# Performance work log

Measured on AMD Instinct MI355X. Metric: run time of the kernel, lower is better.

## Reference

```python
import jax, jax.numpy as jnp
import numpy as np

N, E, H, G, NF, L = 50000, 600000, 128, 50, 128, 6
NC, NM = 500, 100  # conformers, molecules
CUTOFF = 10.0
OFFSET = jnp.linspace(0.0, CUTOFF, G)                 # GaussianSmearing offsets
COEFF = -0.5 / (CUTOFF / (G - 1)) ** 2
LOG2 = float(np.log(2.0))

def ssp(x):  # ShiftedSoftplus
    return jax.nn.softplus(x) - LOG2

def setup_inputs() -> dict:
    key = jax.random.key(0)
    ks = jax.random.split(key, 24)
    s = 0.05
    return {
        'z': jax.random.randint(ks[0], (N,), 0, 120),
        'pos': jax.random.normal(ks[1], (N, 3), jnp.float32) * 5.0,
        'edge_row': jax.random.randint(ks[2], (E,), 0, N),   # source j
        'edge_col': jax.random.randint(ks[3], (E,), 0, N),   # target i
        'atom_to_conf': jnp.sort(jax.random.randint(ks[4], (N,), 0, NC)),
        'conf_to_mol': jnp.sort(jax.random.randint(ks[5], (NC,), 0, NM)),
        'emb_table': jax.random.normal(ks[6], (120, H)) * s,
        'mlp_w1': jax.random.normal(ks[7], (L, G, NF)) * s,
        'mlp_b1': jnp.zeros((L, NF)),
        'mlp_w2': jax.random.normal(ks[8], (L, NF, NF)) * s,
        'mlp_b2': jnp.zeros((L, NF)),
        'conv_lin1_w': jax.random.normal(ks[9], (L, H, NF)) * s,
        'conv_lin2_w': jax.random.normal(ks[10], (L, NF, H)) * s,
        'conv_lin2_b': jnp.zeros((L, H)),
        'int_lin_w': jax.random.normal(ks[11], (L, H, H)) * s,
        'int_lin_b': jnp.zeros((L, H)),
        'lin1_w': jax.random.normal(ks[12], (H, H)) * s,
        'lin1_b': jnp.zeros((H,)),
        'lin2_w': jax.random.normal(ks[13], (H, H)) * s,
        'lin2_b': jnp.zeros((H,)),
        'head_w1': jax.random.normal(ks[14], (H, H // 2)) * s,
        'head_b1': jnp.zeros((H // 2,)),
        'head_w2': jax.random.normal(ks[15], (H // 2, 1)) * s,
        'head_b2': jnp.zeros((1,)),
    }

def reference(z, pos, edge_row, edge_col, atom_to_conf, conf_to_mol,
              emb_table, mlp_w1, mlp_b1, mlp_w2, mlp_b2,
              conv_lin1_w, conv_lin2_w, conv_lin2_b, int_lin_w, int_lin_b,
              lin1_w, lin1_b, lin2_w, lin2_b,
              head_w1, head_b1, head_w2, head_b2):
    h = emb_table[z]                                         # [N,H]
    # edge geometry (radius graph distances)
    d = jnp.linalg.norm(pos[edge_row] - pos[edge_col], axis=-1)       # [E]
    edge_attr = jnp.exp(COEFF * (d[:, None] - OFFSET[None, :]) ** 2)  # [E,G]
    C = 0.5 * (jnp.cos(d * jnp.pi / CUTOFF) + 1.0)                    # [E]
    for i in range(L):
        # filter network + cosine cutoff
        W = ssp(edge_attr @ mlp_w1[i] + mlp_b1[i]) @ mlp_w2[i] + mlp_b2[i]
        W = W * C[:, None]                                   # [E,NF]
        xf = h @ conv_lin1_w[i]                              # [N,NF]
        msg = xf[edge_row] * W                               # gather x_j, multiply
        agg = jax.ops.segment_sum(msg, edge_col, num_segments=N)  # scatter-add
        x = agg @ conv_lin2_w[i] + conv_lin2_b[i]
        x = ssp(x) @ int_lin_w[i] + int_lin_b[i]
        h = h + x                                            # residual
    h = ssp(h @ lin1_w + lin1_b) @ lin2_w + lin2_b           # [N,H]
    conf_emb = jax.ops.segment_sum(h, atom_to_conf, num_segments=NC)  # [NC,H]
    mol_emb = jax.ops.segment_sum(conf_emb, conf_to_mol, num_segments=NM)  # [NM,H]
    out = (ssp(mol_emb @ head_w1 + head_b1) @ head_w2 + head_b2)[:, 0]  # [NM]
    return out
```

## Files before the change

kernel.cpp:

```cpp
#include <hip/hip_runtime.h>
#include <hip/hip_bf16.h>
#include <hip/hip_fp16.h>
#include <math.h>

#define H_DIM   128
#define NF_DIM  128
#define G_DIM   50
#define L_LAYERS 6
#define TBL     4096
#define DMAX    12.8f
#define CUTOFF_C 10.0f
#define COEFF_C (-0.5f * 49.0f * 49.0f / 100.0f)
#define SCAN_B  256
#define T_PER   16
#define STG_STR 140

typedef __bf16 bf16x8 __attribute__((ext_vector_type(8)));
typedef float  f32x4  __attribute__((ext_vector_type(4)));

__device__ __forceinline__ float sspf(float x) {
    float e = __expf(-fabsf(x));
    return fmaxf(x, 0.0f) + __logf(1.0f + e) - 0.69314718055994530942f;
}

__device__ __forceinline__ unsigned short f2bf(float f) {
    unsigned int u = __float_as_uint(f);
    u = (u + 0x7fffu + ((u >> 16) & 1u)) >> 16;
    return (unsigned short)u;
}

__device__ __forceinline__ float bf2f(unsigned short u) {
    return __uint_as_float(((unsigned int)u) << 16);
}

__device__ __forceinline__ int swz(int c) {
    return c ^ ((c >> 3) & 7) ^ ((c >> 8) & 3);
}

__global__ __launch_bounds__(128) void bt_sy(
        const float* __restrict__ w1, const float* __restrict__ b1,
        unsigned short* __restrict__ syb) {
    int l  = blockIdx.x / (TBL / T_PER);
    int t0 = (blockIdx.x % (TBL / T_PER)) * T_PER;
    int f  = threadIdx.x;
    __shared__ float sW1[G_DIM * 128];
    __shared__ float gs[T_PER][G_DIM + 2];
    for (int i = f; i < G_DIM * 128; i += 128)
        sW1[i] = w1[(size_t)l * G_DIM * 128 + i];
    if (f < G_DIM) {
        float o = f * (CUTOFF_C / (G_DIM - 1));
#pragma unroll
        for (int u = 0; u < T_PER; ++u) {
            float dt = (t0 + u) * (DMAX / (TBL - 1));
            float dd = dt - o;
            gs[u][f] = __expf(COEFF_C * dd * dd);
        }
    }
    __syncthreads();
    float y[T_PER];
    float bb = b1[l * 128 + f];
#pragma unroll
    for (int u = 0; u < T_PER; ++u) y[u] = bb;
    for (int g = 0; g < G_DIM; ++g) {
        float wv = sW1[g * 128 + f];
#pragma unroll
        for (int u = 0; u < T_PER; ++u) y[u] += gs[u][g] * wv;
    }
#pragma unroll
    for (int u = 0; u < T_PER; ++u)
        syb[((size_t)l * TBL + t0 + u) * 128 + f] = f2bf(sspf(y[u]));
}

__global__ __launch_bounds__(256, 4) void bt_gemm(
        const unsigned short* __restrict__ syb, const unsigned short* __restrict__ w2sw,
        const float* __restrict__ b2, unsigned short* __restrict__ tabb) {
    int l  = blockIdx.x >> 6;
    int m0 = (blockIdx.x & 63) * 64;
    const unsigned short* A = syb + (size_t)l * TBL * 128;
    const unsigned short* Bsw = w2sw + (size_t)l * 16384;
    const float* bias = b2 + l * 128;
    unsigned short* outp = tabb + (size_t)l * TBL * 128;

    __shared__ __align__(16) unsigned short frag[8192];
    __shared__ __align__(16) unsigned short stg[64 * STG_STR];
    int tid = threadIdx.x;
    for (int i = tid; i < 1024; i += 256) {
        int ks = i >> 8, w_ = (i >> 6) & 3, ln_ = i & 63;
        int row = m0 + w_ * 16 + (ln_ & 15);
        int kb = ks * 32 + (ln_ >> 4) * 8;
        uint4 v = *(const uint4*)(A + (size_t)row * 128 + kb);
        *(uint4*)(frag + swz(i) * 8) = v;
    }
    __syncthreads();
    int w = tid >> 6, ln = tid & 63;
    int quad = ln >> 4, l15 = ln & 15;
    f32x4 acc[8] = {};
#pragma unroll
    for (int ks = 0; ks < 4; ++ks) {
        bf16x8 af = *(const bf16x8*)(frag + swz((ks * 4 + w) * 64 + ln) * 8);
#pragma unroll
        for (int j = 0; j < 8; ++j) {
            bf16x8 bf = *(const bf16x8*)(Bsw + (((ks * 8 + j) * 64) + ln) * 8);
            acc[j] = __builtin_amdgcn_mfma_f32_16x16x32_bf16(af, bf, acc[j], 0, 0, 0);
        }
    }
#pragma unroll
    for (int j = 0; j < 8; ++j) {
        int col = j * 16 + l15;
        float bv = bias[col];
#pragma unroll
        for (int r = 0; r < 4; ++r)
            stg[(w * 16 + quad * 4 + r) * STG_STR + col] = f2bf(acc[j][r] + bv);
    }
    __syncthreads();
    for (int i = tid; i < 2048; i += 256) {
        int row = i >> 5, c4 = (i & 31) * 4;
        ushort4 s4 = *(const ushort4*)(stg + row * STG_STR + c4);
        *(uint2*)(outp + (size_t)(m0 + row) * 128 + c4) = *(const uint2*)&s4;
    }
}

__global__ __launch_bounds__(256) void embed_kernel(
        const int* __restrict__ z, const float* __restrict__ emb,
        unsigned short* __restrict__ hb, int N) {
    int idx = blockIdx.x * blockDim.x + threadIdx.x;
    if (idx >= N * H_DIM) return;
    int n = idx >> 7, f = idx & 127;
    hb[idx] = f2bf(emb[z[n] * H_DIM + f]);
}

__global__ __launch_bounds__(256) void prep_wt_all(
        const float* __restrict__ c1w, const float* __restrict__ c2w,
        const float* __restrict__ iw, const float* __restrict__ l1w,
        const float* __restrict__ w2, unsigned short* __restrict__ Bsw) {
    int m = blockIdx.x;
    const float* src = (m < 6)  ? c1w + (size_t)m * 16384
                     : (m < 12) ? c2w + (size_t)(m - 6) * 16384
                     : (m < 18) ? iw  + (size_t)(m - 12) * 16384
                     : (m == 18) ? l1w
                                 : w2 + (size_t)(m - 19) * 16384;
    unsigned short* dst = Bsw + (size_t)m * 16384;
    for (int i = threadIdx.x; i < 16384; i += 256) {
        int jj = i & 7, lane = (i >> 3) & 63, j = (i >> 9) & 7, ks = i >> 12;
        int n = j * 16 + (lane & 15);
        int k = ks * 32 + ((lane >> 4) & 3) * 8 + jj;
        dst[i] = f2bf(src[k * 128 + n]);
    }
}

__global__ __launch_bounds__(256) void count_kernel(
        const int* __restrict__ ec, int* __restrict__ cnt,
        int* __restrict__ rank, int E) {
    int e = blockIdx.x * blockDim.x + threadIdx.x;
    if (e < E) rank[e] = atomicAdd(&cnt[ec[e]], 1);
}

__global__ __launch_bounds__(SCAN_B) void scan1(
        const int* __restrict__ cnt, int* __restrict__ excl,
        int* __restrict__ bsums, int N) {
    __shared__ int s[SCAN_B];
    int i = blockIdx.x * SCAN_B + threadIdx.x;
    int v = (i < N) ? cnt[i] : 0;
    s[threadIdx.x] = v;
    __syncthreads();
    for (int off = 1; off < SCAN_B; off <<= 1) {
        int t = (threadIdx.x >= off) ? s[threadIdx.x - off] : 0;
        __syncthreads();
        s[threadIdx.x] += t;
        __syncthreads();
    }
    if (i < N) excl[i] = s[threadIdx.x] - v;
    if (threadIdx.x == SCAN_B - 1) bsums[blockIdx.x] = s[SCAN_B - 1];
}

__global__ __launch_bounds__(SCAN_B) void scan2(int* __restrict__ bsums, int nb) {
    __shared__ int s[SCAN_B];
    int v = (threadIdx.x < nb) ? bsums[threadIdx.x] : 0;
    s[threadIdx.x] = v;
    __syncthreads();
    for (int off = 1; off < SCAN_B; off <<= 1) {
        int t = (threadIdx.x >= off) ? s[threadIdx.x - off] : 0;
        __syncthreads();
        s[threadIdx.x] += t;
        __syncthreads();
    }
    if (threadIdx.x < nb) bsums[threadIdx.x] = s[threadIdx.x] - v;
}

__global__ __launch_bounds__(SCAN_B) void scan3(
        const int* __restrict__ excl, const int* __restrict__ bsums,
        int* __restrict__ row_start, int N, int E) {
    int i = blockIdx.x * SCAN_B + threadIdx.x;
    if (i < N) row_start[i] = excl[i] + bsums[blockIdx.x];
    if (i == 0) row_start[N] = E;
}

__global__ __launch_bounds__(256) void build_edges(
        const int* __restrict__ er, const int* __restrict__ ec,
        const float* __restrict__ pos, const int* __restrict__ row_start,
        const int* __restrict__ rank, uint2* __restrict__ ebuf, int E) {
    int e = blockIdx.x * blockDim.x + threadIdx.x;
    if (e >= E) return;
    int r = er[e], c = ec[e];
    float dx = pos[r * 3 + 0] - pos[c * 3 + 0];
    float dy = pos[r * 3 + 1] - pos[c * 3 + 1];
    float dz = pos[r * 3 + 2] - pos[c * 3 + 2];
    float d = sqrtf(dx * dx + dy * dy + dz * dz);
    float C = 0.5f * (cosf(d * (3.14159265358979323846f / CUTOFF_C)) + 1.0f);
    float t = fminf(d, DMAX) * ((TBL - 1) / DMAX);
    int i0 = (int)(t + 0.5f);
    if (i0 > TBL - 1) i0 = TBL - 1;
    ebuf[row_start[c] + rank[e]] =
        make_uint2((unsigned)r | ((unsigned)i0 << 17), __float_as_uint(C));
}

__device__ __forceinline__ void edge_acc(
        unsigned ex, unsigned ey, const unsigned short* __restrict__ tabb,
        const unsigned short* __restrict__ xfb, int f4, float4& acc) {
    int r = ex & 0x1ffff, i0 = ex >> 17;
    float C = __uint_as_float(ey);
    const ushort4 tw = *(const ushort4*)(tabb + (size_t)i0 * 128 + f4);
    const ushort4 xu = *(const ushort4*)(xfb + (size_t)r * 128 + f4);
    acc.x = fmaf(bf2f(xu.x) * bf2f(tw.x), C, acc.x);
    acc.y = fmaf(bf2f(xu.y) * bf2f(tw.y), C, acc.y);
    acc.z = fmaf(bf2f(xu.z) * bf2f(tw.z), C, acc.z);
    acc.w = fmaf(bf2f(xu.w) * bf2f(tw.w), C, acc.w);
}

__global__ __launch_bounds__(256) void edge_agg(
        const uint2* __restrict__ ebuf, const int* __restrict__ row_start,
        const unsigned short* __restrict__ xfb, const unsigned short* __restrict__ tabb,
        unsigned short* __restrict__ aggb, int N) {
    int tid = threadIdx.x;
    int atom = blockIdx.x * 8 + (tid >> 5);
    if (atom >= N) return;
    int f4 = (tid & 31) * 4;
    float4 a0 = make_float4(0.f, 0.f, 0.f, 0.f);
    float4 a1 = make_float4(0.f, 0.f, 0.f, 0.f);
    float4 a2 = make_float4(0.f, 0.f, 0.f, 0.f);
    float4 a3 = make_float4(0.f, 0.f, 0.f, 0.f);
    int j0 = row_start[atom], j1 = row_start[atom + 1];
    int j = j0;
    if (j < j1 && (j & 1)) {
        uint2 ed = ebuf[j];
        edge_acc(ed.x, ed.y, tabb, xfb, f4, a0);
        ++j;
    }
    for (; j + 3 < j1; j += 4) {
        uint4 e0 = *(const uint4*)(ebuf + j);
        uint4 e1 = *(const uint4*)(ebuf + j + 2);
        edge_acc(e0.x, e0.y, tabb, xfb, f4, a0);
        edge_acc(e0.z, e0.w, tabb, xfb, f4, a1);
        edge_acc(e1.x, e1.y, tabb, xfb, f4, a2);
        edge_acc(e1.z, e1.w, tabb, xfb, f4, a3);
    }
    if (j + 1 < j1) {
        uint4 e0 = *(const uint4*)(ebuf + j);
        edge_acc(e0.x, e0.y, tabb, xfb, f4, a0);
        edge_acc(e0.z, e0.w, tabb, xfb, f4, a1);
        j += 2;
    }
    if (j < j1) {
        uint2 ed = ebuf[j];
        edge_acc(ed.x, ed.y, tabb, xfb, f4, a0);
    }
    a0.x += a1.x + a2.x + a3.x;
    a0.y += a1.y + a2.y + a3.y;
    a0.z += a1.z + a2.z + a3.z;
    a0.w += a1.w + a2.w + a3.w;
    unsigned short o[4] = {f2bf(a0.x), f2bf(a0.y), f2bf(a0.z), f2bf(a0.w)};
    *(uint2*)(aggb + (size_t)atom * 128 + f4) = *(const uint2*)o;
}

__global__ __launch_bounds__(256, 4) void gemm_l0(
        const unsigned short* __restrict__ hb, const unsigned short* __restrict__ Bsw,
        unsigned short* __restrict__ xfb, int M) {
    __shared__ __align__(16) unsigned short frag[8192];
    __shared__ __align__(16) unsigned short stg[64 * STG_STR];
    int tid = threadIdx.x;
    int m0 = blockIdx.x * 64;
    for (int i = tid; i < 1024; i += 256) {
        int ks = i >> 8, w_ = (i >> 6) & 3, ln_ = i & 63;
        int row = m0 + w_ * 16 + (ln_ & 15);
        int kb = ks * 32 + (ln_ >> 4) * 8;
        uint4 v = make_uint4(0, 0, 0, 0);
        if (row < M) v = *(const uint4*)(hb + (size_t)row * 128 + kb);
        *(uint4*)(frag + swz(i) * 8) = v;
    }
    __syncthreads();
    int w = tid >> 6, ln = tid & 63;
    int quad = ln >> 4, l15 = ln & 15;
    f32x4 acc[8] = {};
#pragma unroll
    for (int ks = 0; ks < 4; ++ks) {
        bf16x8 af = *(const bf16x8*)(frag + swz((ks * 4 + w) * 64 + ln) * 8);
#pragma unroll
        for (int j = 0; j < 8; ++j) {
            bf16x8 bf = *(const bf16x8*)(Bsw + (((ks * 8 + j) * 64) + ln) * 8);
            acc[j] = __builtin_amdgcn_mfma_f32_16x16x32_bf16(af, bf, acc[j], 0, 0, 0);
        }
    }
#pragma unroll
    for (int j = 0; j < 8; ++j) {
        int col = j * 16 + l15;
#pragma unroll
        for (int r = 0; r < 4; ++r)
            stg[(w * 16 + quad * 4 + r) * STG_STR + col] = f2bf(acc[j][r]);
    }
    __syncthreads();
    for (int i = tid; i < 2048; i += 256) {
        int row = i >> 5, c4 = (i & 31) * 4;
        int grow = m0 + row;
        if (grow >= M) continue;
        ushort4 s4 = *(const ushort4*)(stg + row * STG_STR + c4);
        *(uint2*)(xfb + (size_t)grow * 128 + c4) = *(const uint2*)&s4;
    }
}

__global__ __launch_bounds__(256, 4) void fused_layer(
        const unsigned short* __restrict__ aggb,
        const unsigned short* __restrict__ B1sw, const float* __restrict__ b1v,
        const unsigned short* __restrict__ B2sw, const float* __restrict__ b2v,
        const unsigned short* __restrict__ B3sw, const float* __restrict__ b3v,
        unsigned short* __restrict__ hb, unsigned short* __restrict__ xfb_next,
        float* __restrict__ s_out, int M, int last) {
    __shared__ __align__(16) unsigned short frag[8192];
    __shared__ __align__(16) unsigned short stg[64 * STG_STR];
    int tid = threadIdx.x;
    int m0 = blockIdx.x * 64;

    for (int i = tid; i < 1024; i += 256) {
        int ks = i >> 8, w_ = (i >> 6) & 3, ln_ = i & 63;
        int row = m0 + w_ * 16 + (ln_ & 15);
        int kb = ks * 32 + (ln_ >> 4) * 8;
        uint4 v = make_uint4(0, 0, 0, 0);
        if (row < M) v = *(const uint4*)(aggb + (size_t)row * 128 + kb);
        *(uint4*)(frag + swz(i) * 8) = v;
    }
    __syncthreads();

    int w = tid >> 6, ln = tid & 63;
    int quad = ln >> 4, l15 = ln & 15;

    f32x4 acc[8] = {};
#pragma unroll
    for (int ks = 0; ks < 4; ++ks) {
        bf16x8 af = *(const bf16x8*)(frag + swz((ks * 4 + w) * 64 + ln) * 8);
#pragma unroll
        for (int j = 0; j < 8; ++j) {
            bf16x8 bf = *(const bf16x8*)(B1sw + (((ks * 8 + j) * 64) + ln) * 8);
            acc[j] = __builtin_amdgcn_mfma_f32_16x16x32_bf16(af, bf, acc[j], 0, 0, 0);
        }
    }

#pragma unroll
    for (int j = 0; j < 8; ++j) {
        int col = j * 16 + l15;
        float bv = b1v[col];
        int ks2 = j >> 1;
        int quad2 = (col >> 3) & 3;
        int jj = l15 & 7;
        int cbase = (ks2 * 4 + w) * 64 + quad2 * 16 + quad * 4;
#pragma unroll
        for (int r = 0; r < 4; ++r) {
            float s = sspf(acc[j][r] + bv);
            frag[swz(cbase + r) * 8 + jj] = f2bf(s);
        }
    }

    f32x4 acc2[8] = {};
#pragma unroll
    for (int ks = 0; ks < 4; ++ks) {
        bf16x8 af = *(const bf16x8*)(frag + swz((ks * 4 + w) * 64 + ln) * 8);
#pragma unroll
        for (int j = 0; j < 8; ++j) {
            bf16x8 bf = *(const bf16x8*)(B2sw + (((ks * 8 + j) * 64) + ln) * 8);
            acc2[j] = __builtin_amdgcn_mfma_f32_16x16x32_bf16(af, bf, acc2[j], 0, 0, 0);
        }
    }

#pragma unroll
    for (int j = 0; j < 8; ++j) {
        int col = j * 16 + l15;
        float bv = b2v[col];
#pragma unroll
        for (int r = 0; r < 4; ++r)
            stg[(w * 16 + quad * 4 + r) * STG_STR + col] = f2bf(acc2[j][r] + bv);
    }
    __syncthreads();

    for (int i = tid; i < 2048; i += 256) {
        int row = i >> 5, c4 = (i & 31) * 4;
        int grow = m0 + row;
        ushort4 xv = *(const ushort4*)(stg + row * STG_STR + c4);
        unsigned short t4[4];
        if (grow < M) {
            unsigned short* hp = hb + (size_t)grow * 128 + c4;
            ushort4 hv = *(const ushort4*)hp;
            t4[0] = f2bf(bf2f(hv.x) + bf2f(xv.x));
            t4[1] = f2bf(bf2f(hv.y) + bf2f(xv.y));
            t4[2] = f2bf(bf2f(hv.z) + bf2f(xv.z));
            t4[3] = f2bf(bf2f(hv.w) + bf2f(xv.w));
            *(uint2*)hp = *(const uint2*)t4;
        } else {
            t4[0] = t4[1] = t4[2] = t4[3] = 0;
        }
        int w_ = row >> 4, l15_ = row & 15;
        int ks = c4 >> 5, q_ = (c4 >> 3) & 3, jj = c4 & 7;
        int c = (ks * 4 + w_) * 64 + q_ * 16 + l15_;
        *(uint2*)(frag + swz(c) * 8 + jj) = *(const uint2*)t4;
    }
    __syncthreads();

    f32x4 acc3[8] = {};
#pragma unroll
    for (int ks = 0; ks < 4; ++ks) {
        bf16x8 af = *(const bf16x8*)(frag + swz((ks * 4 + w) * 64 + ln) * 8);
#pragma unroll
        for (int j = 0; j < 8; ++j) {
            bf16x8 bf = *(const bf16x8*)(B3sw + (((ks * 8 + j) * 64) + ln) * 8);
            acc3[j] = __builtin_amdgcn_mfma_f32_16x16x32_bf16(af, bf, acc3[j], 0, 0, 0);
        }
    }

#pragma unroll
    for (int j = 0; j < 8; ++j) {
        int col = j * 16 + l15;
        float bv = last ? b3v[col] : 0.f;
#pragma unroll
        for (int r = 0; r < 4; ++r) {
            float v = acc3[j][r] + bv;
            if (last) v = sspf(v);
            stg[(w * 16 + quad * 4 + r) * STG_STR + col] = f2bf(v);
        }
    }
    __syncthreads();

    for (int i = tid; i < 2048; i += 256) {
        int row = i >> 5, c4 = (i & 31) * 4;
        int grow = m0 + row;
        if (grow >= M) continue;
        ushort4 s4 = *(const ushort4*)(stg + row * STG_STR + c4);
        if (last) {
            float4 v;
            v.x = bf2f(s4.x); v.y = bf2f(s4.y); v.z = bf2f(s4.z); v.w = bf2f(s4.w);
            *(float4*)(s_out + (size_t)grow * 128 + c4) = v;
        } else {
            *(uint2*)(xfb_next + (size_t)grow * 128 + c4) = *(const uint2*)&s4;
        }
    }
}

#define MR_ATOMS 32
__global__ __launch_bounds__(128) void mol_reduce(
        const float* __restrict__ s, const int* __restrict__ a2c,
        const int* __restrict__ c2m, float* __restrict__ mols,
        int* __restrict__ cnt, int N) {
    int f = threadIdx.x;
    int a0 = blockIdx.x * MR_ATOMS;
    int a1 = min(a0 + MR_ATOMS, N);
    float sum = 0.f;
    int cur = -1, run = 0;
    for (int a = a0; a < a1; ++a) {
        int m = c2m[a2c[a]];
        if (m != cur) {
            if (cur >= 0) {
                unsafeAtomicAdd(&mols[(size_t)cur * H_DIM + f], sum);
                if (f == 0) atomicAdd(&cnt[cur], run);
            }
            cur = m; sum = 0.f; run = 0;
        }
        sum += s[(size_t)a * H_DIM + f];
        ++run;
    }
    if (cur >= 0) {
        unsafeAtomicAdd(&mols[(size_t)cur * H_DIM + f], sum);
        if (f == 0) atomicAdd(&cnt[cur], run);
    }
}

__global__ __launch_bounds__(128) void head_kernel(
        const float* __restrict__ mols, const int* __restrict__ cnt,
        const float* __restrict__ l2w, const float* __restrict__ l2b,
        const float* __restrict__ hw1, const float* __restrict__ hb1,
        const float* __restrict__ hw2, const float* __restrict__ hb2,
        float* __restrict__ out) {
    int m = blockIdx.x, f = threadIdx.x;
    __shared__ float me[H_DIM];
    __shared__ float u[H_DIM / 2];
    const float* ms = mols + (size_t)m * H_DIM;
    float acc = l2b[f] * (float)cnt[m];
#pragma unroll 16
    for (int k = 0; k < H_DIM; ++k) acc += ms[k] * l2w[k * H_DIM + f];
    me[f] = acc;
    __syncthreads();
    if (f < 64) {
        float a2 = hb1[f];
#pragma unroll 16
        for (int k = 0; k < H_DIM; ++k) a2 += me[k] * hw1[k * 64 + f];
        u[f] = sspf(a2);
    }
    __syncthreads();
    if (f == 0) {
        float o = hb2[0];
#pragma unroll 16
        for (int j = 0; j < 64; ++j) o += u[j] * hw2[j];
        out[m] = o;
    }
}

extern "C" void kernel_launch(void* const* d_in, const int* in_sizes, int n_in,
                              void* d_out, int out_size, void* d_ws, size_t ws_size,
                              hipStream_t stream) {
    const int*   z   = (const int*)d_in[0];
    const float* pos = (const float*)d_in[1];
    const int*   er  = (const int*)d_in[2];
    const int*   ec  = (const int*)d_in[3];
    const int*   a2c = (const int*)d_in[4];
    const int*   c2m = (const int*)d_in[5];
    const float* emb = (const float*)d_in[6];
    const float* w1  = (const float*)d_in[7];
    const float* b1  = (const float*)d_in[8];
    const float* w2  = (const float*)d_in[9];
    const float* b2  = (const float*)d_in[10];
    const float* c1w = (const float*)d_in[11];
    const float* c2w = (const float*)d_in[12];
    const float* c2b = (const float*)d_in[13];
    const float* iw  = (const float*)d_in[14];
    const float* ib  = (const float*)d_in[15];
    const float* l1w = (const float*)d_in[16];
    const float* l1b = (const float*)d_in[17];
    const float* l2w = (const float*)d_in[18];
    const float* l2b = (const float*)d_in[19];
    const float* hw1 = (const float*)d_in[20];
    const float* hb1 = (const float*)d_in[21];
    const float* hw2 = (const float*)d_in[22];
    const float* hb2 = (const float*)d_in[23];

    const int N  = in_sizes[0];
    const int E  = in_sizes[2];
    const int NM = out_size;
    float* out = (float*)d_out;

    char* wsp = (char*)d_ws;
    uint2* ebuf = (uint2*)wsp;            wsp += (size_t)E * 8;
    unsigned short* tabb = (unsigned short*)wsp;  wsp += (size_t)L_LAYERS * TBL * NF_DIM * 2;
    unsigned short* syb  = (unsigned short*)wsp;  wsp += (size_t)L_LAYERS * TBL * NF_DIM * 2;
    unsigned short* wbt = (unsigned short*)wsp;  wsp += (size_t)25 * 16384 * 2;
    unsigned short* hb  = (unsigned short*)wsp;  wsp += (size_t)N * H_DIM * 2;
    unsigned short* xfb = (unsigned short*)wsp;  wsp += (size_t)N * H_DIM * 2;
    unsigned short* aggb = (unsigned short*)wsp; wsp += (size_t)N * H_DIM * 2;
    float* sbuf = (float*)wsp;            wsp += (size_t)N * H_DIM * 4;
    float* mols = (float*)wsp;            wsp += (size_t)NM * H_DIM * 4;
    int*   cnt_m = (int*)wsp;             wsp += (size_t)NM * 4;
    int*   ccnt  = (int*)wsp;             wsp += (size_t)N * 4;
    int*   row_start = (int*)wsp;         wsp += (size_t)(N + 1) * 4;
    int*   rank  = (int*)wsp;             wsp += (size_t)E * 4;
    int*   bsums = (int*)wsp;             wsp += 256 * 4;
    int*   excl  = (int*)wsp;

    hipMemsetAsync(ccnt, 0, (size_t)N * sizeof(int), stream);
    count_kernel<<<(E + 255) / 256, 256, 0, stream>>>(ec, ccnt, rank, E);
    int nb = (N + SCAN_B - 1) / SCAN_B;
    scan1<<<nb, SCAN_B, 0, stream>>>(ccnt, excl, bsums, N);
    scan2<<<1, SCAN_B, 0, stream>>>(bsums, nb);
    scan3<<<nb, SCAN_B, 0, stream>>>(excl, bsums, row_start, N, E);
    build_edges<<<(E + 255) / 256, 256, 0, stream>>>(
        er, ec, pos, row_start, rank, ebuf, E);

    bt_sy<<<L_LAYERS * (TBL / T_PER), 128, 0, stream>>>(w1, b1, syb);
    embed_kernel<<<(N * H_DIM + 255) / 256, 256, 0, stream>>>(z, emb, hb, N);
    prep_wt_all<<<25, 256, 0, stream>>>(c1w, c2w, iw, l1w, w2, wbt);
    bt_gemm<<<L_LAYERS * (TBL / 64), 256, 0, stream>>>(
        syb, wbt + (size_t)19 * 16384, b2, tabb);

    int gblocks = (N + 63) / 64;
    gemm_l0<<<gblocks, 256, 0, stream>>>(hb, wbt, xfb, N);

    for (int l = 0; l < L_LAYERS; ++l) {
        edge_agg<<<(N + 7) / 8, 256, 0, stream>>>(
            ebuf, row_start, xfb, tabb + (size_t)l * TBL * NF_DIM, aggb, N);
        int last = (l == L_LAYERS - 1);
        const unsigned short* B3 = last ? wbt + (size_t)18 * 16384
                                        : wbt + (size_t)(l + 1) * 16384;
        fused_layer<<<gblocks, 256, 0, stream>>>(
            aggb,
            wbt + (size_t)(6 + l) * 16384,  c2b + (size_t)l * H_DIM,
            wbt + (size_t)(12 + l) * 16384, ib + (size_t)l * H_DIM,
            B3, l1b, hb, xfb, sbuf, N, last);
    }

    hipMemsetAsync(mols, 0, (size_t)NM * H_DIM * sizeof(float) + NM * sizeof(int), stream);
    mol_reduce<<<(N + MR_ATOMS - 1) / MR_ATOMS, 128, 0, stream>>>(
        sbuf, a2c, c2m, mols, cnt_m, N);
    head_kernel<<<NM, 128, 0, stream>>>(mols, cnt_m, l2w, l2b, hw1, hb1, hw2, hb2, out);
}
```

Baseline: 618.9 us.

## Fuse edge aggregation into the per-layer GEMM kernel and ping-pong xf buffers

Edge gather/aggregation now runs inside fused_layer. Each 64-atom block accumulates its messages and writes them straight into the swizzled LDS fragment layout, so the separate edge_agg launch and the aggb global round-trip go away. The xf buffers ping-pong because the next layer's xf is written while other blocks still read the current one. The last layer now stores bf16 instead of fp32, and mol_reduce reads bf16. The trade-off is fewer blocks per layer for the gather phase (64 atoms per block instead of 8) and GEMM work serialized behind irregular gathers inside one block.

New measurement: 656.7 us. 6.1% more time.

```diff
diff --git a/kernel.cpp b/kernel.cpp
--- a/kernel.cpp
+++ b/kernel.cpp
@@ -227,51 +227,6 @@
     acc.w = fmaf(bf2f(xu.w) * bf2f(tw.w), C, acc.w);
 }
 
-__global__ __launch_bounds__(256) void edge_agg(
-        const uint2* __restrict__ ebuf, const int* __restrict__ row_start,
-        const unsigned short* __restrict__ xfb, const unsigned short* __restrict__ tabb,
-        unsigned short* __restrict__ aggb, int N) {
-    int tid = threadIdx.x;
-    int atom = blockIdx.x * 8 + (tid >> 5);
-    if (atom >= N) return;
-    int f4 = (tid & 31) * 4;
-    float4 a0 = make_float4(0.f, 0.f, 0.f, 0.f);
-    float4 a1 = make_float4(0.f, 0.f, 0.f, 0.f);
-    float4 a2 = make_float4(0.f, 0.f, 0.f, 0.f);
-    float4 a3 = make_float4(0.f, 0.f, 0.f, 0.f);
-    int j0 = row_start[atom], j1 = row_start[atom + 1];
-    int j = j0;
-    if (j < j1 && (j & 1)) {
-        uint2 ed = ebuf[j];
-        edge_acc(ed.x, ed.y, tabb, xfb, f4, a0);
-        ++j;
-    }
-    for (; j + 3 < j1; j += 4) {
-        uint4 e0 = *(const uint4*)(ebuf + j);
-        uint4 e1 = *(const uint4*)(ebuf + j + 2);
-        edge_acc(e0.x, e0.y, tabb, xfb, f4, a0);
-        edge_acc(e0.z, e0.w, tabb, xfb, f4, a1);
-        edge_acc(e1.x, e1.y, tabb, xfb, f4, a2);
-        edge_acc(e1.z, e1.w, tabb, xfb, f4, a3);
-    }
-    if (j + 1 < j1) {
-        uint4 e0 = *(const uint4*)(ebuf + j);
-        edge_acc(e0.x, e0.y, tabb, xfb, f4, a0);
-        edge_acc(e0.z, e0.w, tabb, xfb, f4, a1);
-        j += 2;
-    }
-    if (j < j1) {
-        uint2 ed = ebuf[j];
-        edge_acc(ed.x, ed.y, tabb, xfb, f4, a0);
-    }
-    a0.x += a1.x + a2.x + a3.x;
-    a0.y += a1.y + a2.y + a3.y;
-    a0.z += a1.z + a2.z + a3.z;
-    a0.w += a1.w + a2.w + a3.w;
-    unsigned short o[4] = {f2bf(a0.x), f2bf(a0.y), f2bf(a0.z), f2bf(a0.w)};
-    *(uint2*)(aggb + (size_t)atom * 128 + f4) = *(const uint2*)o;
-}
-
 __global__ __launch_bounds__(256, 4) void gemm_l0(
         const unsigned short* __restrict__ hb, const unsigned short* __restrict__ Bsw,
         unsigned short* __restrict__ xfb, int M) {
@@ -318,24 +273,62 @@
 }
 
 __global__ __launch_bounds__(256, 4) void fused_layer(
-        const unsigned short* __restrict__ aggb,
+        const uint2* __restrict__ ebuf, const int* __restrict__ row_start,
+        const unsigned short* __restrict__ xfb_in, const unsigned short* __restrict__ tabb_l,
         const unsigned short* __restrict__ B1sw, const float* __restrict__ b1v,
         const unsigned short* __restrict__ B2sw, const float* __restrict__ b2v,
         const unsigned short* __restrict__ B3sw, const float* __restrict__ b3v,
-        unsigned short* __restrict__ hb, unsigned short* __restrict__ xfb_next,
-        float* __restrict__ s_out, int M, int last) {
+        unsigned short* __restrict__ hb, unsigned short* __restrict__ xfb_out,
+        int M, int last) {
     __shared__ __align__(16) unsigned short frag[8192];
     __shared__ __align__(16) unsigned short stg[64 * STG_STR];
     int tid = threadIdx.x;
     int m0 = blockIdx.x * 64;
 
-    for (int i = tid; i < 1024; i += 256) {
-        int ks = i >> 8, w_ = (i >> 6) & 3, ln_ = i & 63;
-        int row = m0 + w_ * 16 + (ln_ & 15);
-        int kb = ks * 32 + (ln_ >> 4) * 8;
-        uint4 v = make_uint4(0, 0, 0, 0);
-        if (row < M) v = *(const uint4*)(aggb + (size_t)row * 128 + kb);
-        *(uint4*)(frag + swz(i) * 8) = v;
+    int f4 = (tid & 31) * 4;
+    for (int p = 0; p < 8; ++p) {
+        int row = p * 8 + (tid >> 5);
+        int atom = m0 + row;
+        float4 a0 = make_float4(0.f, 0.f, 0.f, 0.f);
+        float4 a1 = make_float4(0.f, 0.f, 0.f, 0.f);
+        float4 a2 = make_float4(0.f, 0.f, 0.f, 0.f);
+        float4 a3 = make_float4(0.f, 0.f, 0.f, 0.f);
+        if (atom < M) {
+            int j0 = row_start[atom], j1 = row_start[atom + 1];
+            int j = j0;
+            if (j < j1 && (j & 1)) {
+                uint2 ed = ebuf[j];
+                edge_acc(ed.x, ed.y, tabb_l, xfb_in, f4, a0);
+                ++j;
+            }
+            for (; j + 3 < j1; j += 4) {
+                uint4 e0 = *(const uint4*)(ebuf + j);
+                uint4 e1 = *(const uint4*)(ebuf + j + 2);
+                edge_acc(e0.x, e0.y, tabb_l, xfb_in, f4, a0);
+                edge_acc(e0.z, e0.w, tabb_l, xfb_in, f4, a1);
+                edge_acc(e1.x, e1.y, tabb_l, xfb_in, f4, a2);
+                edge_acc(e1.z, e1.w, tabb_l, xfb_in, f4, a3);
+            }
+            if (j + 1 < j1) {
+                uint4 e0 = *(const uint4*)(ebuf + j);
+                edge_acc(e0.x, e0.y, tabb_l, xfb_in, f4, a0);
+                edge_acc(e0.z, e0.w, tabb_l, xfb_in, f4, a1);
+                j += 2;
+            }
+            if (j < j1) {
+                uint2 ed = ebuf[j];
+                edge_acc(ed.x, ed.y, tabb_l, xfb_in, f4, a0);
+            }
+        }
+        a0.x += a1.x + a2.x + a3.x;
+        a0.y += a1.y + a2.y + a3.y;
+        a0.z += a1.z + a2.z + a3.z;
+        a0.w += a1.w + a2.w + a3.w;
+        unsigned short o[4] = {f2bf(a0.x), f2bf(a0.y), f2bf(a0.z), f2bf(a0.w)};
+        int w_ = row >> 4, l15_ = row & 15;
+        int ks = f4 >> 5, q_ = (f4 >> 3) & 3, jj = f4 & 7;
+        int c = (ks * 4 + w_) * 64 + q_ * 16 + l15_;
+        *(uint2*)(frag + swz(c) * 8 + jj) = *(const uint2*)o;
     }
     __syncthreads();
 
@@ -441,19 +434,13 @@
         int grow = m0 + row;
         if (grow >= M) continue;
         ushort4 s4 = *(const ushort4*)(stg + row * STG_STR + c4);
-        if (last) {
-            float4 v;
-            v.x = bf2f(s4.x); v.y = bf2f(s4.y); v.z = bf2f(s4.z); v.w = bf2f(s4.w);
-            *(float4*)(s_out + (size_t)grow * 128 + c4) = v;
-        } else {
-            *(uint2*)(xfb_next + (size_t)grow * 128 + c4) = *(const uint2*)&s4;
-        }
+        *(uint2*)(xfb_out + (size_t)grow * 128 + c4) = *(const uint2*)&s4;
     }
 }
 
 #define MR_ATOMS 32
 __global__ __launch_bounds__(128) void mol_reduce(
-        const float* __restrict__ s, const int* __restrict__ a2c,
+        const unsigned short* __restrict__ s, const int* __restrict__ a2c,
         const int* __restrict__ c2m, float* __restrict__ mols,
         int* __restrict__ cnt, int N) {
     int f = threadIdx.x;
@@ -470,7 +457,7 @@
             }
             cur = m; sum = 0.f; run = 0;
         }
-        sum += s[(size_t)a * H_DIM + f];
+        sum += bf2f(s[(size_t)a * H_DIM + f]);
         ++run;
     }
     if (cur >= 0) {
@@ -548,9 +535,8 @@
     unsigned short* syb  = (unsigned short*)wsp;  wsp += (size_t)L_LAYERS * TBL * NF_DIM * 2;
     unsigned short* wbt = (unsigned short*)wsp;  wsp += (size_t)25 * 16384 * 2;
     unsigned short* hb  = (unsigned short*)wsp;  wsp += (size_t)N * H_DIM * 2;
-    unsigned short* xfb = (unsigned short*)wsp;  wsp += (size_t)N * H_DIM * 2;
-    unsigned short* aggb = (unsigned short*)wsp; wsp += (size_t)N * H_DIM * 2;
-    float* sbuf = (float*)wsp;            wsp += (size_t)N * H_DIM * 4;
+    unsigned short* xfa = (unsigned short*)wsp;  wsp += (size_t)N * H_DIM * 2;
+    unsigned short* xfbb = (unsigned short*)wsp; wsp += (size_t)N * H_DIM * 2;
     float* mols = (float*)wsp;            wsp += (size_t)NM * H_DIM * 4;
     int*   cnt_m = (int*)wsp;             wsp += (size_t)NM * 4;
     int*   ccnt  = (int*)wsp;             wsp += (size_t)N * 4;
@@ -575,23 +561,24 @@
         syb, wbt + (size_t)19 * 16384, b2, tabb);
 
     int gblocks = (N + 63) / 64;
-    gemm_l0<<<gblocks, 256, 0, stream>>>(hb, wbt, xfb, N);
-
+    gemm_l0<<<gblocks, 256, 0, stream>>>(hb, wbt, xfa, N);
+
+    unsigned short* xin = xfa;
+    unsigned short* xout = xfbb;
     for (int l = 0; l < L_LAYERS; ++l) {
-        edge_agg<<<(N + 7) / 8, 256, 0, stream>>>(
-            ebuf, row_start, xfb, tabb + (size_t)l * TBL * NF_DIM, aggb, N);
         int last = (l == L_LAYERS - 1);
         const unsigned short* B3 = last ? wbt + (size_t)18 * 16384
                                         : wbt + (size_t)(l + 1) * 16384;
         fused_layer<<<gblocks, 256, 0, stream>>>(
-            aggb,
+            ebuf, row_start, xin, tabb + (size_t)l * TBL * NF_DIM,
             wbt + (size_t)(6 + l) * 16384,  c2b + (size_t)l * H_DIM,
             wbt + (size_t)(12 + l) * 16384, ib + (size_t)l * H_DIM,
-            B3, l1b, hb, xfb, sbuf, N, last);
+            B3, l1b, hb, xout, N, last);
+        unsigned short* t = xin; xin = xout; xout = t;
     }
 
     hipMemsetAsync(mols, 0, (size_t)NM * H_DIM * sizeof(float) + NM * sizeof(int), stream);
     mol_reduce<<<(N + MR_ATOMS - 1) / MR_ATOMS, 128, 0, stream>>>(
-        sbuf, a2c, c2m, mols, cnt_m, N);
+        xin, a2c, c2m, mols, cnt_m, N);
     head_kernel<<<NM, 128, 0, stream>>>(mols, cnt_m, l2w, l2b, hw1, hb1, hw2, hb2, out);
 }
```
